# Performance work log

Hardware: AMD Instinct MI355X
Metric: run time of the kernel (lower is better)

Reference implementation:

```python
import jax, jax.numpy as jnp
import numpy as np

N = 8192      # number of graph nodes
C = 256       # feature_size
D = C // 2    # projection dim


def setup_inputs() -> dict:
    key = jax.random.key(0)
    ks = jax.random.split(key, 10)
    s_in = 1.0 / np.sqrt(C + 3)   # torch Linear default init scale (uniform bound)
    s_r = 1.0 / np.sqrt(D)
    return {
        "landmarks": jax.random.normal(ks[0], (1, N, 3), dtype=jnp.float32),
        "features": jax.random.normal(ks[1], (1, N, C), dtype=jnp.float32),
        # weights stored [in, out]
        "Wi": jax.random.uniform(ks[2], (C + 3, D), jnp.float32, -s_in, s_in),
        "bi": jax.random.uniform(ks[3], (D,), jnp.float32, -s_in, s_in),
        "Wj": jax.random.uniform(ks[4], (C + 3, D), jnp.float32, -s_in, s_in),
        "bj": jax.random.uniform(ks[5], (D,), jnp.float32, -s_in, s_in),
        "Wk": jax.random.uniform(ks[6], (C + 3, D), jnp.float32, -s_in, s_in),
        "bk": jax.random.uniform(ks[7], (D,), jnp.float32, -s_in, s_in),
        "Wr": jax.random.uniform(ks[8], (D, C), jnp.float32, -s_r, s_r),
        "br": jax.random.uniform(ks[9], (C,), jnp.float32, -s_r, s_r),
    }


def reference(landmarks, features, Wi, bi, Wj, bj, Wk, bk, Wr, br):
    # concat coords + features, drop the singleton batch dim: [N, C+3]
    x = jnp.concatenate([landmarks, features], axis=2)[0]
    fi = x @ Wi + bi                       # [N, D]
    fj = x @ Wj + bj                       # [N, D]
    fk = x @ Wk + bk                       # [N, D]
    att = jax.nn.sigmoid(fi @ fj.T)        # [N, N] sigmoid scores (non-softmax)
    att = att / jnp.sum(att, axis=1, keepdims=True)  # row-sum normalize
    out = (att @ fk) @ Wr + br             # [N, C] restored
    return features + out[None]            # residual, back to [1, N, C]
```

## Files before the change

kernel.cpp:

```cpp
#include <hip/hip_runtime.h>
#include <stdint.h>

#define N_NODES 8192
#define KPAD 272
#define OUTC 384

typedef __attribute__((ext_vector_type(8))) short bhalf8;
typedef __attribute__((ext_vector_type(16))) float f32x16;
typedef __attribute__((ext_vector_type(4))) float f32x4;

__device__ inline unsigned short f2bf_rne(float f) {
    unsigned u = __builtin_bit_cast(unsigned, f);
    u += 0x7FFFu + ((u >> 16) & 1u);
    return (unsigned short)(u >> 16);
}

__device__ inline bhalf8 mk8(unsigned a, unsigned b, unsigned c, unsigned d) {
    union { unsigned u[4]; bhalf8 v; } U;
    U.u[0] = a; U.u[1] = b; U.u[2] = c; U.u[3] = d;
    return U.v;
}

#define GLD_TO_LDS(gptr, lptr)                                                              \
    __builtin_amdgcn_global_load_lds((const __attribute__((address_space(1))) void*)(gptr), \
                                     (__attribute__((address_space(3))) void*)(lptr), 16, 0, 0)

__global__ void k_prep(const float* __restrict__ landmarks, const float* __restrict__ features,
                       const float* __restrict__ Wi, const float* __restrict__ bi,
                       const float* __restrict__ Wj, const float* __restrict__ bj,
                       const float* __restrict__ Wk, const float* __restrict__ bk,
                       const float* __restrict__ Wr,
                       unsigned short* __restrict__ xb, unsigned short* __restrict__ WcatT,
                       unsigned short* __restrict__ WrT, float* __restrict__ bcat) {
    int idx = blockIdx.x * 256 + threadIdx.x;
    const int XB_N = N_NODES * KPAD;
    const int WC_N = OUTC * KPAD;
    const int WR_N = 256 * 128;
    if (idx < XB_N) {
        int i = idx / KPAD, kk = idx - i * KPAD;
        float v = 0.f;
        if (kk < 256) v = features[i * 256 + kk];
        else if (kk < 259) v = landmarks[i * 3 + (kk - 256)];
        xb[idx] = f2bf_rne(v);
        return;
    }
    idx -= XB_N;
    if (idx < WC_N) {
        int n = idx / KPAD, kk = idx - n * KPAD;
        int sel = n >> 7, d = n & 127;
        const float* W = (sel == 0) ? Wi : ((sel == 1) ? Wj : Wk);
        float v = 0.f;
        if (kk < 256) v = W[(kk + 3) * 128 + d];
        else if (kk < 259) v = W[(kk - 256) * 128 + d];
        WcatT[idx] = f2bf_rne(v);
        return;
    }
    idx -= WC_N;
    if (idx < WR_N) {
        int c = idx >> 7, d = idx & 127;
        WrT[idx] = f2bf_rne(Wr[d * 256 + c]);
        return;
    }
    idx -= WR_N;
    if (idx < OUTC) {
        float v = (idx < 128) ? bi[idx] : ((idx < 256) ? bj[idx - 128] : bk[idx - 256]);
        bcat[idx] = v;
    }
}

__global__ __launch_bounds__(256) void k_proj(const unsigned short* __restrict__ xb,
                                              const unsigned short* __restrict__ WcatT,
                                              const float* __restrict__ bcat,
                                              unsigned short* __restrict__ fi,
                                              unsigned short* __restrict__ fj,
                                              unsigned short* __restrict__ fkT) {
    const int tid = threadIdx.x;
    const int w = tid >> 6, l = tid & 63, h = l >> 5, ln = l & 31;
    const int i0 = blockIdx.x * 32;
    f32x16 acc[3] = {};
#pragma unroll
    for (int s = 0; s < 17; ++s) {
        bhalf8 a = *(const bhalf8*)(xb + (size_t)(i0 + ln) * KPAD + s * 16 + h * 8);
#pragma unroll
        for (int t = 0; t < 3; ++t) {
            int n = 96 * w + 32 * t + ln;
            bhalf8 b = *(const bhalf8*)(WcatT + (size_t)n * KPAD + s * 16 + h * 8);
            acc[t] = __builtin_amdgcn_mfma_f32_32x32x16_bf16(a, b, acc[t], 0, 0, 0);
        }
    }
#pragma unroll
    for (int t = 0; t < 3; ++t) {
        int n = 96 * w + 32 * t + ln;
        int sel = n >> 7, d = n & 127;
        float bias = bcat[n];
#pragma unroll
        for (int q = 0; q < 4; ++q) {
            int ib = i0 + 8 * q + 4 * h;
            if (sel < 2) {
                unsigned short* dst = sel ? fj : fi;
#pragma unroll
                for (int r = 0; r < 4; ++r)
                    dst[(size_t)(ib + r) * 128 + d] = f2bf_rne(acc[t][4 * q + r] + bias);
            } else {
                ushort4 pk;
                pk.x = f2bf_rne(acc[t][4 * q + 0] + bias);
                pk.y = f2bf_rne(acc[t][4 * q + 1] + bias);
                pk.z = f2bf_rne(acc[t][4 * q + 2] + bias);
                pk.w = f2bf_rne(acc[t][4 * q + 3] + bias);
                *(ushort4*)(fkT + (size_t)d * N_NODES + ib) = pk;
            }
        }
    }
}

__global__ __launch_bounds__(256, 2) void k_attn(const unsigned short* __restrict__ fi,
                                                 const unsigned short* __restrict__ fj,
                                                 const unsigned short* __restrict__ fkT,
                                                 float* __restrict__ num_part,
                                                 float* __restrict__ den_part) {
    __shared__ __align__(16) char smem[65536];
    unsigned short* fj_s = (unsigned short*)smem;
    unsigned short* fk_s = (unsigned short*)(smem + 32768);
    float* bufA = (float*)smem;
    float* bufB = (float*)(smem + 17408);
    float* denb = (float*)(smem + 34816);

    const int tid = threadIdx.x;
    const int w = tid >> 6, l = tid & 63, h = l >> 5, ln = l & 31;
    const int rt = blockIdx.x & 127, jq = blockIdx.x >> 7;
    const int i0 = rt * 64;
    const int jbase = jq * 2048;

    bhalf8 bfi[2][8];
#pragma unroll
    for (int nt = 0; nt < 2; ++nt)
#pragma unroll
        for (int s = 0; s < 8; ++s)
            bfi[nt][s] = *(const bhalf8*)(fi + (size_t)(i0 + nt * 32 + ln) * 128 + s * 16 + h * 8);

    f32x16 acc[8] = {};
    float dacc0 = 0.f, dacc1 = 0.f;

    const int rsub = l >> 4;
    const int cph = l & 15;

    for (int mt = 0; mt < 16; ++mt) {
        const int j0 = jbase + mt * 128;
#pragma unroll
        for (int q = 0; q < 8; ++q) {
            int r = w * 32 + q * 4 + rsub;
            int c = cph ^ (r & 15);
            GLD_TO_LDS(fj + (size_t)(j0 + r) * 128 + c * 8, (char*)fj_s + (w * 32 + q * 4) * 256);
            GLD_TO_LDS(fkT + (size_t)r * N_NODES + j0 + c * 8, (char*)fk_s + (w * 32 + q * 4) * 256);
        }
        __syncthreads();

        f32x16 st0 = {}, st1 = {};
        const int jrow = w * 32 + ln;
#pragma unroll
        for (int s = 0; s < 8; ++s) {
            int c = (s * 2 + h) ^ (jrow & 15);
            bhalf8 af = *(const bhalf8*)((char*)fj_s + jrow * 256 + c * 16);
            st0 = __builtin_amdgcn_mfma_f32_32x32x16_bf16(af, bfi[0][s], st0, 0, 0, 0);
            st1 = __builtin_amdgcn_mfma_f32_32x32x16_bf16(af, bfi[1][s], st1, 0, 0, 0);
        }

        float sv0[16], sv1[16];
#pragma unroll
        for (int r = 0; r < 16; ++r) {
            float x0 = __builtin_amdgcn_rcpf(1.f + __builtin_amdgcn_exp2f(st0[r] * -1.44269504f));
            float x1 = __builtin_amdgcn_rcpf(1.f + __builtin_amdgcn_exp2f(st1[r] * -1.44269504f));
            dacc0 += x0; dacc1 += x1;
            sv0[r] = x0; sv1[r] = x1;
        }
        unsigned p0[8], p1[8], x0v[8], x1v[8];
#pragma unroll
        for (int q = 0; q < 8; ++q) {
            p0[q] = __builtin_amdgcn_perm(__builtin_bit_cast(unsigned, sv0[2 * q + 1]),
                                          __builtin_bit_cast(unsigned, sv0[2 * q]), 0x07060302u);
            p1[q] = __builtin_amdgcn_perm(__builtin_bit_cast(unsigned, sv1[2 * q + 1]),
                                          __builtin_bit_cast(unsigned, sv1[2 * q]), 0x07060302u);
        }
#pragma unroll
        for (int q = 0; q < 8; ++q) {
            x0v[q] = (unsigned)__shfl_xor((int)p0[q], 32, 64);
            x1v[q] = (unsigned)__shfl_xor((int)p1[q], 32, 64);
        }
        bhalf8 fb[2][2];
        if (h == 0) {
            fb[0][0] = mk8(p0[0], p0[1], x0v[0], x0v[1]);
            fb[0][1] = mk8(p0[4], p0[5], x0v[4], x0v[5]);
            fb[1][0] = mk8(p1[0], p1[1], x1v[0], x1v[1]);
            fb[1][1] = mk8(p1[4], p1[5], x1v[4], x1v[5]);
        } else {
            fb[0][0] = mk8(x0v[2], x0v[3], p0[2], p0[3]);
            fb[0][1] = mk8(x0v[6], x0v[7], p0[6], p0[7]);
            fb[1][0] = mk8(x1v[2], x1v[3], p1[2], p1[3]);
            fb[1][1] = mk8(x1v[6], x1v[7], p1[6], p1[7]);
        }
#pragma unroll
        for (int m4 = 0; m4 < 4; ++m4) {
#pragma unroll
            for (int s2 = 0; s2 < 2; ++s2) {
                int row = m4 * 32 + ln;
                int c = (w * 4 + s2 * 2 + h) ^ (row & 15);
                bhalf8 af = *(const bhalf8*)((char*)fk_s + row * 256 + c * 16);
                acc[m4 * 2 + 0] = __builtin_amdgcn_mfma_f32_32x32x16_bf16(af, fb[0][s2], acc[m4 * 2 + 0], 0, 0, 0);
                acc[m4 * 2 + 1] = __builtin_amdgcn_mfma_f32_32x32x16_bf16(af, fb[1][s2], acc[m4 * 2 + 1], 0, 0, 0);
            }
        }
        __syncthreads();
    }

    {
        float o0 = __shfl_xor(dacc0, 32, 64);
        float o1 = __shfl_xor(dacc1, 32, 64);
        dacc0 += o0; dacc1 += o1;
    }
    if (h == 0) {
        denb[w * 64 + ln] = dacc0;
        denb[w * 64 + 32 + ln] = dacc1;
    }

#pragma unroll
    for (int half = 0; half < 2; ++half) {
        __syncthreads();
        if (w < 2) {
            float* buf = w ? bufB : bufA;
#pragma unroll
            for (int m2 = 0; m2 < 2; ++m2) {
                int m4 = half * 2 + m2;
#pragma unroll
                for (int nt = 0; nt < 2; ++nt) {
                    int iloc = nt * 32 + ln;
#pragma unroll
                    for (int q = 0; q < 4; ++q) {
                        int d = m2 * 32 + 8 * q + 4 * h;
                        f32x4 v = {acc[m4 * 2 + nt][4 * q + 0], acc[m4 * 2 + nt][4 * q + 1],
                                   acc[m4 * 2 + nt][4 * q + 2], acc[m4 * 2 + nt][4 * q + 3]};
                        *(f32x4*)(buf + iloc * 68 + d) = v;
                    }
                }
            }
        }
        __syncthreads();
        if (w >= 2) {
            float* buf = (w == 3) ? bufB : bufA;
#pragma unroll
            for (int m2 = 0; m2 < 2; ++m2) {
                int m4 = half * 2 + m2;
#pragma unroll
                for (int nt = 0; nt < 2; ++nt) {
                    int iloc = nt * 32 + ln;
#pragma unroll
                    for (int q = 0; q < 4; ++q) {
                        int d = m2 * 32 + 8 * q + 4 * h;
                        f32x4 old = *(f32x4*)(buf + iloc * 68 + d);
                        f32x4 v = {acc[m4 * 2 + nt][4 * q + 0], acc[m4 * 2 + nt][4 * q + 1],
                                   acc[m4 * 2 + nt][4 * q + 2], acc[m4 * 2 + nt][4 * q + 3]};
                        *(f32x4*)(buf + iloc * 68 + d) = old + v;
                    }
                }
            }
        }
        __syncthreads();
#pragma unroll
        for (int e = 0; e < 4; ++e) {
            int v = e * 256 + tid;
            int iloc = v >> 4;
            int d4 = (v & 15) * 4;
            f32x4 s = *(f32x4*)(bufA + iloc * 68 + d4) + *(f32x4*)(bufB + iloc * 68 + d4);
            *(f32x4*)(num_part + (size_t)(jq * N_NODES + i0 + iloc) * 128 + half * 64 + d4) = s;
        }
    }
    __syncthreads();
    if (tid < 64) {
        den_part[(size_t)jq * N_NODES + i0 + tid] =
            denb[tid] + denb[64 + tid] + denb[128 + tid] + denb[192 + tid];
    }
}

__global__ void k_comb(const float* __restrict__ num_part, const float* __restrict__ den_part,
                       unsigned short* __restrict__ t) {
    int f = blockIdx.x * 256 + threadIdx.x;
    int i = f >> 5, d4 = (f & 31) * 4;
    f32x4 s = {};
    float ds = 0.f;
#pragma unroll
    for (int q = 0; q < 4; ++q) {
        s += *(const f32x4*)(num_part + (size_t)(q * N_NODES + i) * 128 + d4);
        ds += den_part[(size_t)q * N_NODES + i];
    }
    float inv = 1.0f / ds;
    ushort4 pk;
    pk.x = f2bf_rne(s.x * inv);
    pk.y = f2bf_rne(s.y * inv);
    pk.z = f2bf_rne(s.z * inv);
    pk.w = f2bf_rne(s.w * inv);
    *(ushort4*)(t + (size_t)i * 128 + d4) = pk;
}

__global__ __launch_bounds__(256) void k_out(const unsigned short* __restrict__ t,
                                             const unsigned short* __restrict__ WrT,
                                             const float* __restrict__ br,
                                             const float* __restrict__ features,
                                             float* __restrict__ out) {
    __shared__ __align__(16) char smem[65536];
    const int tid = threadIdx.x, w = tid >> 6, l = tid & 63, h = l >> 5, ln = l & 31;
    const int i0 = blockIdx.x * 32;
    {
        int rsub = l >> 4, cph = l & 15;
#pragma unroll
        for (int q = 0; q < 16; ++q) {
            int r = w * 64 + q * 4 + rsub;
            int c = cph ^ (r & 15);
            GLD_TO_LDS(WrT + (size_t)r * 128 + c * 8, (char*)smem + (w * 64 + q * 4) * 256);
        }
    }
    __syncthreads();
    f32x16 acc[2] = {};
#pragma unroll
    for (int s = 0; s < 8; ++s) {
        bhalf8 af = *(const bhalf8*)(t + (size_t)(i0 + ln) * 128 + s * 16 + h * 8);
#pragma unroll
        for (int nt = 0; nt < 2; ++nt) {
            int row = w * 64 + nt * 32 + ln;
            int c = (s * 2 + h) ^ (row & 15);
            bhalf8 bf = *(const bhalf8*)((char*)smem + row * 256 + c * 16);
            acc[nt] = __builtin_amdgcn_mfma_f32_32x32x16_bf16(af, bf, acc[nt], 0, 0, 0);
        }
    }
#pragma unroll
    for (int nt = 0; nt < 2; ++nt) {
        int cc = w * 64 + nt * 32 + ln;
        float bias = br[cc];
#pragma unroll
        for (int q = 0; q < 4; ++q) {
#pragma unroll
            for (int r = 0; r < 4; ++r) {
                int i = i0 + 8 * q + 4 * h + r;
                out[(size_t)i * 256 + cc] = acc[nt][4 * q + r] + bias + features[(size_t)i * 256 + cc];
            }
        }
    }
}

extern "C" void kernel_launch(void* const* d_in, const int* in_sizes, int n_in,
                              void* d_out, int out_size, void* d_ws, size_t ws_size,
                              hipStream_t stream) {
    const float* landmarks = (const float*)d_in[0];
    const float* features  = (const float*)d_in[1];
    const float* Wi = (const float*)d_in[2];
    const float* bi = (const float*)d_in[3];
    const float* Wj = (const float*)d_in[4];
    const float* bj = (const float*)d_in[5];
    const float* Wk = (const float*)d_in[6];
    const float* bk = (const float*)d_in[7];
    const float* Wr = (const float*)d_in[8];
    const float* br = (const float*)d_in[9];

    char* ws = (char*)d_ws;
    unsigned short* xb      = (unsigned short*)(ws + 0);
    unsigned short* WcatT   = (unsigned short*)(ws + 4456448);
    unsigned short* WrT     = (unsigned short*)(ws + 4665344);
    float*          bcat    = (float*)(ws + 4730880);
    unsigned short* fi      = (unsigned short*)(ws + 4732416);
    unsigned short* fjp     = (unsigned short*)(ws + 6829568);
    unsigned short* fkT     = (unsigned short*)(ws + 8926720);
    float*          num_part= (float*)(ws + 11023872);
    float*          den_part= (float*)(ws + 27801088);
    unsigned short* t       = (unsigned short*)(ws + 27932160);

    float* out = (float*)d_out;

    hipLaunchKernelGGL(k_prep, dim3(9242), dim3(256), 0, stream,
                       landmarks, features, Wi, bi, Wj, bj, Wk, bk, Wr, xb, WcatT, WrT, bcat);
    hipLaunchKernelGGL(k_proj, dim3(256), dim3(256), 0, stream, xb, WcatT, bcat, fi, fjp, fkT);
    hipLaunchKernelGGL(k_attn, dim3(512), dim3(256), 0, stream, fi, fjp, fkT, num_part, den_part);
    hipLaunchKernelGGL(k_comb, dim3(1024), dim3(256), 0, stream, num_part, den_part, t);
    hipLaunchKernelGGL(k_out, dim3(256), dim3(256), 0, stream, t, WrT, br, features, out);
}
```

Measured before the change: 183.1 us.

## Widen attention blocks to 128 rows, store bf16 partials, fuse combine into output

The attention kernel now runs 512 threads per block covering 128 query rows. Each 128-column key tile staged in LDS is therefore shared by two row groups, and the key range splits 8 ways instead of 4. Partial numerators are written as bf16 instead of fp32, which halves that traffic. The separate combine kernel is removed: the output kernel now sums the 8 partials, normalizes and stages the result in LDS itself. This trades fewer launches and less global traffic for more partial sums, bf16 rounding of the partials, and possible occupancy pressure from 512-thread blocks with 64KB of LDS.

```diff
diff --git a/kernel.cpp b/kernel.cpp
--- a/kernel.cpp
+++ b/kernel.cpp
@@ -13,6 +13,10 @@
     unsigned u = __builtin_bit_cast(unsigned, f);
     u += 0x7FFFu + ((u >> 16) & 1u);
     return (unsigned short)(u >> 16);
+}
+
+__device__ inline float bf2f(unsigned short u) {
+    return __builtin_bit_cast(float, ((unsigned)u) << 16);
 }
 
 __device__ inline bhalf8 mk8(unsigned a, unsigned b, unsigned c, unsigned d) {
@@ -113,10 +117,10 @@
     }
 }
 
-__global__ __launch_bounds__(256, 2) void k_attn(const unsigned short* __restrict__ fi,
+__global__ __launch_bounds__(512, 4) void k_attn(const unsigned short* __restrict__ fi,
                                                  const unsigned short* __restrict__ fj,
                                                  const unsigned short* __restrict__ fkT,
-                                                 float* __restrict__ num_part,
+                                                 unsigned short* __restrict__ num_part,
                                                  float* __restrict__ den_part) {
     __shared__ __align__(16) char smem[65536];
     unsigned short* fj_s = (unsigned short*)smem;
@@ -127,16 +131,19 @@
 
     const int tid = threadIdx.x;
     const int w = tid >> 6, l = tid & 63, h = l >> 5, ln = l & 31;
-    const int rt = blockIdx.x & 127, jq = blockIdx.x >> 7;
-    const int i0 = rt * 64;
-    const int jbase = jq * 2048;
+    const int g = w & 3;
+    const int ih = w >> 2;
+    const int rt = blockIdx.x >> 3, jq = blockIdx.x & 7;
+    const int i0 = rt * 128;
+    const int ibase = i0 + ih * 64;
+    const int jbase = jq * 1024;
 
     bhalf8 bfi[2][8];
 #pragma unroll
     for (int nt = 0; nt < 2; ++nt)
 #pragma unroll
         for (int s = 0; s < 8; ++s)
-            bfi[nt][s] = *(const bhalf8*)(fi + (size_t)(i0 + nt * 32 + ln) * 128 + s * 16 + h * 8);
+            bfi[nt][s] = *(const bhalf8*)(fi + (size_t)(ibase + nt * 32 + ln) * 128 + s * 16 + h * 8);
 
     f32x16 acc[8] = {};
     float dacc0 = 0.f, dacc1 = 0.f;
@@ -144,19 +151,21 @@
     const int rsub = l >> 4;
     const int cph = l & 15;
 
-    for (int mt = 0; mt < 16; ++mt) {
+    for (int mt = 0; mt < 8; ++mt) {
         const int j0 = jbase + mt * 128;
 #pragma unroll
         for (int q = 0; q < 8; ++q) {
-            int r = w * 32 + q * 4 + rsub;
+            int r = g * 32 + q * 4 + rsub;
             int c = cph ^ (r & 15);
-            GLD_TO_LDS(fj + (size_t)(j0 + r) * 128 + c * 8, (char*)fj_s + (w * 32 + q * 4) * 256);
-            GLD_TO_LDS(fkT + (size_t)r * N_NODES + j0 + c * 8, (char*)fk_s + (w * 32 + q * 4) * 256);
+            if (w < 4)
+                GLD_TO_LDS(fj + (size_t)(j0 + r) * 128 + c * 8, (char*)fj_s + (g * 32 + q * 4) * 256);
+            else
+                GLD_TO_LDS(fkT + (size_t)r * N_NODES + j0 + c * 8, (char*)fk_s + (g * 32 + q * 4) * 256);
         }
         __syncthreads();
 
         f32x16 st0 = {}, st1 = {};
-        const int jrow = w * 32 + ln;
+        const int jrow = g * 32 + ln;
 #pragma unroll
         for (int s = 0; s < 8; ++s) {
             int c = (s * 2 + h) ^ (jrow & 15);
@@ -203,7 +212,7 @@
 #pragma unroll
             for (int s2 = 0; s2 < 2; ++s2) {
                 int row = m4 * 32 + ln;
-                int c = (w * 4 + s2 * 2 + h) ^ (row & 15);
+                int c = (g * 4 + s2 * 2 + h) ^ (row & 15);
                 bhalf8 af = *(const bhalf8*)((char*)fk_s + row * 256 + c * 16);
                 acc[m4 * 2 + 0] = __builtin_amdgcn_mfma_f32_32x32x16_bf16(af, fb[0][s2], acc[m4 * 2 + 0], 0, 0, 0);
                 acc[m4 * 2 + 1] = __builtin_amdgcn_mfma_f32_32x32x16_bf16(af, fb[1][s2], acc[m4 * 2 + 1], 0, 0, 0);
@@ -223,89 +232,79 @@
     }
 
 #pragma unroll
-    for (int half = 0; half < 2; ++half) {
-        __syncthreads();
-        if (w < 2) {
-            float* buf = w ? bufB : bufA;
-#pragma unroll
-            for (int m2 = 0; m2 < 2; ++m2) {
-                int m4 = half * 2 + m2;
-#pragma unroll
-                for (int nt = 0; nt < 2; ++nt) {
-                    int iloc = nt * 32 + ln;
-#pragma unroll
-                    for (int q = 0; q < 4; ++q) {
-                        int d = m2 * 32 + 8 * q + 4 * h;
-                        f32x4 v = {acc[m4 * 2 + nt][4 * q + 0], acc[m4 * 2 + nt][4 * q + 1],
-                                   acc[m4 * 2 + nt][4 * q + 2], acc[m4 * 2 + nt][4 * q + 3]};
-                        *(f32x4*)(buf + iloc * 68 + d) = v;
+    for (int g2 = 0; g2 < 2; ++g2) {
+#pragma unroll
+        for (int half = 0; half < 2; ++half) {
+            __syncthreads();
+            if (ih == g2 && (w & 3) < 2) {
+                float* buf = (w & 3) ? bufB : bufA;
+#pragma unroll
+                for (int m2 = 0; m2 < 2; ++m2) {
+                    int m4 = half * 2 + m2;
+#pragma unroll
+                    for (int nt = 0; nt < 2; ++nt) {
+                        int iloc = nt * 32 + ln;
+#pragma unroll
+                        for (int q = 0; q < 4; ++q) {
+                            int d = m2 * 32 + 8 * q + 4 * h;
+                            f32x4 v = {acc[m4 * 2 + nt][4 * q + 0], acc[m4 * 2 + nt][4 * q + 1],
+                                       acc[m4 * 2 + nt][4 * q + 2], acc[m4 * 2 + nt][4 * q + 3]};
+                            *(f32x4*)(buf + iloc * 68 + d) = v;
+                        }
                     }
                 }
             }
-        }
-        __syncthreads();
-        if (w >= 2) {
-            float* buf = (w == 3) ? bufB : bufA;
-#pragma unroll
-            for (int m2 = 0; m2 < 2; ++m2) {
-                int m4 = half * 2 + m2;
-#pragma unroll
-                for (int nt = 0; nt < 2; ++nt) {
-                    int iloc = nt * 32 + ln;
-#pragma unroll
-                    for (int q = 0; q < 4; ++q) {
-                        int d = m2 * 32 + 8 * q + 4 * h;
-                        f32x4 old = *(f32x4*)(buf + iloc * 68 + d);
-                        f32x4 v = {acc[m4 * 2 + nt][4 * q + 0], acc[m4 * 2 + nt][4 * q + 1],
-                                   acc[m4 * 2 + nt][4 * q + 2], acc[m4 * 2 + nt][4 * q + 3]};
-                        *(f32x4*)(buf + iloc * 68 + d) = old + v;
+            __syncthreads();
+            if (ih == g2 && (w & 3) >= 2) {
+                float* buf = ((w & 3) == 3) ? bufB : bufA;
+#pragma unroll
+                for (int m2 = 0; m2 < 2; ++m2) {
+                    int m4 = half * 2 + m2;
+#pragma unroll
+                    for (int nt = 0; nt < 2; ++nt) {
+                        int iloc = nt * 32 + ln;
+#pragma unroll
+                        for (int q = 0; q < 4; ++q) {
+                            int d = m2 * 32 + 8 * q + 4 * h;
+                            f32x4 old = *(f32x4*)(buf + iloc * 68 + d);
+                            f32x4 v = {acc[m4 * 2 + nt][4 * q + 0], acc[m4 * 2 + nt][4 * q + 1],
+                                       acc[m4 * 2 + nt][4 * q + 2], acc[m4 * 2 + nt][4 * q + 3]};
+                            *(f32x4*)(buf + iloc * 68 + d) = old + v;
+                        }
                     }
                 }
             }
-        }
-        __syncthreads();
-#pragma unroll
-        for (int e = 0; e < 4; ++e) {
-            int v = e * 256 + tid;
-            int iloc = v >> 4;
-            int d4 = (v & 15) * 4;
-            f32x4 s = *(f32x4*)(bufA + iloc * 68 + d4) + *(f32x4*)(bufB + iloc * 68 + d4);
-            *(f32x4*)(num_part + (size_t)(jq * N_NODES + i0 + iloc) * 128 + half * 64 + d4) = s;
+            __syncthreads();
+#pragma unroll
+            for (int e = 0; e < 2; ++e) {
+                int v = e * 512 + tid;
+                int iloc = v >> 4;
+                int d4 = (v & 15) * 4;
+                f32x4 s = *(f32x4*)(bufA + iloc * 68 + d4) + *(f32x4*)(bufB + iloc * 68 + d4);
+                ushort4 pk;
+                pk.x = f2bf_rne(s.x); pk.y = f2bf_rne(s.y);
+                pk.z = f2bf_rne(s.z); pk.w = f2bf_rne(s.w);
+                *(ushort4*)(num_part + (size_t)(jq * N_NODES + i0 + g2 * 64 + iloc) * 128 + half * 64 + d4) = pk;
+            }
         }
     }
     __syncthreads();
-    if (tid < 64) {
-        den_part[(size_t)jq * N_NODES + i0 + tid] =
-            denb[tid] + denb[64 + tid] + denb[128 + tid] + denb[192 + tid];
-    }
-}
-
-__global__ void k_comb(const float* __restrict__ num_part, const float* __restrict__ den_part,
-                       unsigned short* __restrict__ t) {
-    int f = blockIdx.x * 256 + threadIdx.x;
-    int i = f >> 5, d4 = (f & 31) * 4;
-    f32x4 s = {};
-    float ds = 0.f;
-#pragma unroll
-    for (int q = 0; q < 4; ++q) {
-        s += *(const f32x4*)(num_part + (size_t)(q * N_NODES + i) * 128 + d4);
-        ds += den_part[(size_t)q * N_NODES + i];
-    }
-    float inv = 1.0f / ds;
-    ushort4 pk;
-    pk.x = f2bf_rne(s.x * inv);
-    pk.y = f2bf_rne(s.y * inv);
-    pk.z = f2bf_rne(s.z * inv);
-    pk.w = f2bf_rne(s.w * inv);
-    *(ushort4*)(t + (size_t)i * 128 + d4) = pk;
-}
-
-__global__ __launch_bounds__(256) void k_out(const unsigned short* __restrict__ t,
+    if (tid < 128) {
+        int ihh = tid >> 6, t = tid & 63;
+        den_part[(size_t)jq * N_NODES + i0 + ihh * 64 + t] =
+            denb[(ihh * 4 + 0) * 64 + t] + denb[(ihh * 4 + 1) * 64 + t] +
+            denb[(ihh * 4 + 2) * 64 + t] + denb[(ihh * 4 + 3) * 64 + t];
+    }
+}
+
+__global__ __launch_bounds__(256) void k_out(const unsigned short* __restrict__ num_part,
+                                             const float* __restrict__ den_part,
                                              const unsigned short* __restrict__ WrT,
                                              const float* __restrict__ br,
                                              const float* __restrict__ features,
                                              float* __restrict__ out) {
-    __shared__ __align__(16) char smem[65536];
+    __shared__ __align__(16) char smem[73728];
+    unsigned short* t_s = (unsigned short*)(smem + 65536);
     const int tid = threadIdx.x, w = tid >> 6, l = tid & 63, h = l >> 5, ln = l & 31;
     const int i0 = blockIdx.x * 32;
     {
@@ -317,11 +316,34 @@
             GLD_TO_LDS(WrT + (size_t)r * 128 + c * 8, (char*)smem + (w * 64 + q * 4) * 256);
         }
     }
+#pragma unroll
+    for (int e = 0; e < 2; ++e) {
+        int v = e * 256 + tid;
+        int r = v >> 4, c8 = v & 15;
+        float s[8] = {};
+        float den = 0.f;
+#pragma unroll
+        for (int q = 0; q < 8; ++q) {
+            const unsigned short* p = num_part + (size_t)(q * N_NODES + i0 + r) * 128 + c8 * 8;
+            union { uint4 u; unsigned short us[8]; } U;
+            U.u = *(const uint4*)p;
+#pragma unroll
+            for (int z = 0; z < 8; ++z) s[z] += bf2f(U.us[z]);
+            den += den_part[(size_t)q * N_NODES + i0 + r];
+        }
+        float inv = 1.0f / den;
+        union { ushort4 a[2]; uint4 u; } P;
+#pragma unroll
+        for (int z = 0; z < 8; ++z) ((unsigned short*)&P)[z] = f2bf_rne(s[z] * inv);
+        int pc = c8 ^ (r & 15);
+        *(uint4*)((char*)t_s + r * 256 + pc * 16) = P.u;
+    }
     __syncthreads();
     f32x16 acc[2] = {};
 #pragma unroll
     for (int s = 0; s < 8; ++s) {
-        bhalf8 af = *(const bhalf8*)(t + (size_t)(i0 + ln) * 128 + s * 16 + h * 8);
+        int ca = (s * 2 + h) ^ (ln & 15);
+        bhalf8 af = *(const bhalf8*)((char*)t_s + ln * 256 + ca * 16);
 #pragma unroll
         for (int nt = 0; nt < 2; ++nt) {
             int row = w * 64 + nt * 32 + ln;
@@ -367,16 +389,14 @@
     unsigned short* fi      = (unsigned short*)(ws + 4732416);
     unsigned short* fjp     = (unsigned short*)(ws + 6829568);
     unsigned short* fkT     = (unsigned short*)(ws + 8926720);
-    float*          num_part= (float*)(ws + 11023872);
+    unsigned short* num_part= (unsigned short*)(ws + 11023872);
     float*          den_part= (float*)(ws + 27801088);
-    unsigned short* t       = (unsigned short*)(ws + 27932160);
 
     float* out = (float*)d_out;
 
     hipLaunchKernelGGL(k_prep, dim3(9242), dim3(256), 0, stream,
                        landmarks, features, Wi, bi, Wj, bj, Wk, bk, Wr, xb, WcatT, WrT, bcat);
     hipLaunchKernelGGL(k_proj, dim3(256), dim3(256), 0, stream, xb, WcatT, bcat, fi, fjp, fkT);
-    hipLaunchKernelGGL(k_attn, dim3(512), dim3(256), 0, stream, fi, fjp, fkT, num_part, den_part);
-    hipLaunchKernelGGL(k_comb, dim3(1024), dim3(256), 0, stream, num_part, den_part, t);
-    hipLaunchKernelGGL(k_out, dim3(256), dim3(256), 0, stream, t, WrT, br, features, out);
-}
+    hipLaunchKernelGGL(k_attn, dim3(512), dim3(512), 0, stream, fi, fjp, fkT, num_part, den_part);
+    hipLaunchKernelGGL(k_out, dim3(256), dim3(256), 0, stream, num_part, den_part, WrT, br, features, out);
+}
```

Result: slower. 434.4 us (+137.3%).
